# Optimization experiments

Measured on AMD Instinct MI355X. Metric: run time of the kernel, lower is better.

Reference implementation:

```python
import jax, jax.numpy as jnp
import numpy as np

EPS = 1e-8
LRELU_SLOPE = 0.2
ACT_GAIN = float(np.sqrt(2.0))  # def_gain for lrelu
GAIN = 1.0                      # forward default
CLAMP = 256.0


def setup_inputs() -> dict:
    key = jax.random.key(0)
    k1, k2 = jax.random.split(key)
    x = jax.random.normal(k1, (8, 128, 32, 32, 32), dtype=jnp.float32)
    weight = jax.random.normal(k2, (128, 128, 3, 3, 3), dtype=jnp.float32)
    bias = jnp.zeros((128,), dtype=jnp.float32)
    return {"x": x, "weight": weight, "bias": bias}


def _modulated_conv3d(x, weight, styles, padding, demodulate=True):
    # x: [B, Cin, D, H, W], weight: [Cout, Cin, kd, kh, kw], styles: [B, Cin]
    w = weight[None] * styles[:, None, :, None, None, None]  # [B, Cout, Cin, kd, kh, kw]
    if demodulate:
        dcoefs = jax.lax.rsqrt(jnp.sum(jnp.square(w), axis=(2, 3, 4, 5)) + EPS)  # [B, Cout]
        w = w * dcoefs[:, :, None, None, None, None]
    pad = [(padding, padding)] * 3

    def per_sample(xi, wi):
        # xi: [Cin, D, H, W], wi: [Cout, Cin, kd, kh, kw]
        return jax.lax.conv_general_dilated(
            xi[None], wi, window_strides=(1, 1, 1), padding=pad,
            dimension_numbers=("NCDHW", "OIDHW", "NCDHW"))[0]

    return jax.vmap(per_sample)(x, w)  # [B, Cout, D, H, W]


def reference(x, weight, bias):
    padding = weight.shape[-1] // 2
    styles = jnp.ones((x.shape[0], weight.shape[1]), dtype=x.dtype)
    y = _modulated_conv3d(x, weight, styles, padding)
    y = jax.nn.leaky_relu(y + bias[None, :, None, None, None], LRELU_SLOPE)
    # clamp_gain(act, act_gain*gain, 256*gain)
    return jnp.clip(y * (ACT_GAIN * GAIN), -CLAMP * GAIN, CLAMP * GAIN)
```

## Files before the change

### kernel.cpp

```cpp
#include <hip/hip_runtime.h>

typedef short bf16x8 __attribute__((ext_vector_type(8)));
typedef float f32x4  __attribute__((ext_vector_type(4)));
typedef unsigned short u16;

static __device__ __forceinline__ u16 f2bf(float f) {
    unsigned int u = __builtin_bit_cast(unsigned int, f);
    u += 0x7FFFu + ((u >> 16) & 1u);
    return (u16)(u >> 16);
}

static __device__ __forceinline__ void gload_lds16(const void* g, void* l) {
    __builtin_amdgcn_global_load_lds((const __attribute__((address_space(1))) void*)g,
                                     (__attribute__((address_space(3))) void*)l, 16, 0, 0);
}

__global__ __launch_bounds__(256) void prep_w_k(const float* __restrict__ w,
                                                u16* __restrict__ wn) {
    const int co = blockIdx.x;
    const int t  = threadIdx.x;
    const float* wc = w + co * 3456;
    float s = 0.f;
    for (int i = t; i < 3456; i += 256) { float v = wc[i]; s += v * v; }
#pragma unroll
    for (int off = 32; off; off >>= 1) s += __shfl_down(s, off);
    __shared__ float red[4];
    __shared__ float dsh;
    if ((t & 63) == 0) red[t >> 6] = s;
    __syncthreads();
    if (t == 0) dsh = rsqrtf(red[0] + red[1] + red[2] + red[3] + 1e-8f);
    __syncthreads();
    const float d = dsh;
    for (int i = t; i < 3456; i += 256) {
        int ci = i / 27, tap = i - ci * 27;
        float v = wc[i] * d;
        wn[((tap * 4 + (ci >> 5)) * 128 + co) * 32 + (ci & 31)] = f2bf(v);
    }
}

__global__ __launch_bounds__(256) void xpose_k(const float* __restrict__ x,
                                               u16* __restrict__ xt) {
    const int bid = blockIdx.x;
    const int b = bid >> 10, d = (bid >> 5) & 31, h = bid & 31;
    const int t = threadIdx.x;
    const int w = t & 31, cg = t >> 5;
    const int base_dhw = d * 1024 + h * 32 + w;
#pragma unroll
    for (int r = 0; r < 2; ++r) {
        int g = cg + r * 8;
        const float* src = x + ((size_t)(b * 128 + g * 8) << 15) + base_dhw;
        bf16x8 pk;
#pragma unroll
        for (int j = 0; j < 8; ++j) pk[j] = (short)f2bf(src[(size_t)j << 15]);
        *(bf16x8*)&xt[((size_t)((b * 16 + g) << 15) + base_dhw) * 8] = pk;
    }
}

#define KSX 1048576
#define KSW 4096
__global__ __launch_bounds__(512, 4) void conv_mx(
    const u16* __restrict__ wsb, const float* __restrict__ bias,
    float* __restrict__ out) {
    __shared__ __align__(16) u16 lds[24576];
    const u16* xt = wsb + 524288;
    const u16* wn = wsb + 512;
    const u16* zp = wsb;

    const int t = threadIdx.x, lane = t & 63, wid = t >> 6;
    const int ll = lane & 15, g = lane >> 4;
    const int mslice = wid >> 1, ncol = wid & 1;

    int wg = ((blockIdx.x & 7) << 7) | (blockIdx.x >> 3);
    const int b = wg >> 7, dt = (wg >> 3) & 15, ht = wg & 7;
    const int d0 = dt * 2, h0 = ht * 4;

    const int pos0 = mslice * 64 + ll;
    const int xro = pos0 * 32 + ((g ^ ((pos0 >> 1) & 3)) * 8);
    const int co0 = ncol * 64 + ll;
    const int wro = 16384 + co0 * 32 + ((g ^ ((co0 >> 1) & 3)) * 8);

    const int posA = wid * 32 + (lane >> 2);
    const int slot = lane & 3;
    const int pdA = posA >> 7, phA = (posA >> 5) & 3, wA = posA & 31;
    const int gA = slot ^ ((posA >> 1) & 3);
    const int wco = wid * 16 + (lane >> 2);
    const u16* wsrc = wn + wco * 32 + ((slot ^ ((wco >> 1) & 3)) * 8);

    f32x4 acc[4][4];
#pragma unroll
    for (int i = 0; i < 4; ++i)
#pragma unroll
        for (int j = 0; j < 4; ++j) acc[i][j] = (f32x4){0.f, 0.f, 0.f, 0.f};

    const u16* xs0; bool okA, okB;
    const u16* xn0; bool nkA, nkB;

#define MKADDR(OD, OH, OW, A0, OA, OB) { \
    int Dx = d0 + pdA - 1 + (OD), Hx = h0 + phA - 1 + (OH), Wx = wA - 1 + (OW); \
    bool dh_ = ((unsigned)Dx < 32u) && ((unsigned)Hx < 32u); \
    OA = dh_ && ((unsigned)Wx < 32u); \
    OB = dh_ && (Wx < 16); \
    A0 = xt + (long)((b * 16 + gA) * 32768 + Dx * 1024 + Hx * 32 + Wx) * 8; }

#define STAGE(A0, OA, OB, PAR) { \
    gload_lds16(OA ? (const void*)(A0) : (const void*)zp, (void*)&lds[(PAR)*8192 + wid*1024]); \
    gload_lds16(OB ? (const void*)((A0) + 128) : (const void*)zp, (void*)&lds[(PAR)*8192 + wid*1024 + 512]); \
    gload_lds16((const void*)wsrc, (void*)&lds[16384 + (PAR)*4096 + wid*512]); \
    A0 += KSX; wsrc += KSW; }

#define FRAGMFMA(PAR) { \
    bf16x8 xf[4], wf[4]; \
    _Pragma("unroll") for (int mf = 0; mf < 4; ++mf) \
        xf[mf] = *(const bf16x8*)&lds[xro + (PAR)*8192 + mf*512]; \
    _Pragma("unroll") for (int nf = 0; nf < 4; ++nf) \
        wf[nf] = *(const bf16x8*)&lds[wro + (PAR)*4096 + nf*512]; \
    __builtin_amdgcn_s_setprio(1); \
    _Pragma("unroll") for (int mf = 0; mf < 4; ++mf) \
    _Pragma("unroll") for (int nf = 0; nf < 4; ++nf) \
        acc[mf][nf] = __builtin_amdgcn_mfma_f32_16x16x32_bf16(wf[nf], xf[mf], acc[mf][nf], 0, 0, 0); \
    __builtin_amdgcn_s_setprio(0); }

    MKADDR(0, 0, 0, xs0, okA, okB);
    STAGE(xs0, okA, okB, 0);
    __syncthreads();

    for (int od = 0; od < 3; ++od)
    for (int oh = 0; oh < 3; ++oh)
    for (int ow = 0; ow < 3; ++ow) {
        const bool last = (od == 2) && (oh == 2) && (ow == 2);
        STAGE(xs0, okA, okB, 1);
        FRAGMFMA(0);
        __syncthreads();
        STAGE(xs0, okA, okB, 0);
        {
            int own = (ow < 2) ? ow + 1 : 0;
            int ohn = (ow < 2) ? oh : ((oh < 2) ? oh + 1 : 0);
            int odn = (ow < 2) ? od : ((oh < 2) ? od : od + 1);
            MKADDR(odn, ohn, own, xn0, nkA, nkB);
        }
        FRAGMFMA(1);
        __syncthreads();
        STAGE(xs0, okA, okB, 1);
        FRAGMFMA(0);
        __syncthreads();
        if (!last) { STAGE(xn0, nkA, nkB, 0); }
        FRAGMFMA(1);
        __syncthreads();
        xs0 = xn0; okA = nkA; okB = nkB;
    }

    const int pd = mslice >> 1, phb = (mslice & 1) * 2;
#pragma unroll
    for (int nf = 0; nf < 4; ++nf) {
        f32x4 bb = *(const f32x4*)&bias[ncol * 64 + nf * 16 + g * 4];
#pragma unroll
        for (int mf = 0; mf < 4; ++mf) {
            const int wq = (mf & 1) * 16 + ll;
            const int hh = h0 + phb + (mf >> 1);
            float* orow = out + ((size_t)(b * 128 + ncol * 64 + nf * 16 + g * 4) << 15)
                          + (d0 + pd) * 1024 + hh * 32 + wq;
#pragma unroll
            for (int q = 0; q < 4; ++q) {
                float v = acc[mf][nf][q] + bb[q];
                v = v > 0.f ? v : v * 0.2f;
                v *= 1.41421356237f;
                v = fminf(fmaxf(v, -256.f), 256.f);
                orow[(size_t)q << 15] = v;
            }
        }
    }
#undef MKADDR
#undef STAGE
#undef FRAGMFMA
}

#define NPOS 544
__global__ __launch_bounds__(256, 4) void conv_fb(
    const float* __restrict__ x, const u16* __restrict__ wn,
    const float* __restrict__ bias, float* __restrict__ out) {
    __shared__ __align__(16) u16 lds[NPOS * 32];
    float* ldsf = reinterpret_cast<float*>(lds);
    const int t = threadIdx.x;
    const int lane = t & 63;
    const int wid  = t >> 6;
    const int wr   = wid >> 1;
    const int wcn  = wid & 1;
    const int ll   = lane & 15;
    const int g    = lane >> 4;
    const int bid = blockIdx.x;
    const int b  = bid >> 8;
    const int dt = (bid >> 4) & 15, ht = bid & 15;
    const int d0 = dt * 2, h0 = ht * 2;
    const int sw  = t & 31;
    const int sg  = (t >> 5) & 3;
    const int rhi = t >> 7;
    f32x4 acc[4][4];
#pragma unroll
    for (int i = 0; i < 4; ++i)
#pragma unroll
        for (int j = 0; j < 4; ++j) acc[i][j] = (f32x4){0.f, 0.f, 0.f, 0.f};
    float bv[4][4];
#pragma unroll
    for (int nf = 0; nf < 4; ++nf) {
        f32x4 bb = *(const f32x4*)&bias[wcn * 64 + nf * 16 + g * 4];
#pragma unroll
        for (int q = 0; q < 4; ++q) bv[nf][q] = bb[q];
    }
    if (t < 128) {
        int pi  = t >> 2;
        int row = pi >> 1;
        int pos = row * 34 + (pi & 1) * 33;
        bf16x8 z = {0, 0, 0, 0, 0, 0, 0, 0};
        *(bf16x8*)&lds[pos * 32 + (t & 3) * 8] = z;
    }
    for (int c = 0; c < 4; ++c) {
        if (c) __syncthreads();
#pragma unroll
        for (int p = 0; p < 8; ++p) {
            int rowid = p * 2 + rhi;
            int pd = rowid >> 2, ph = rowid & 3;
            int d = d0 - 1 + pd, h = h0 - 1 + ph;
            bool ok = ((unsigned)d < 32u) && ((unsigned)h < 32u);
            const float* src = x + (((b * 128 + c * 32 + sg * 8) * 32 + d) * 32 + h) * 32 + sw;
            float v[8];
#pragma unroll
            for (int j = 0; j < 8; ++j) v[j] = ok ? src[j * 32768] : 0.f;
            bf16x8 pk;
#pragma unroll
            for (int j = 0; j < 8; ++j) pk[j] = (short)f2bf(v[j]);
            int pos = rowid * 34 + sw + 1;
            int sl = sg ^ ((pos >> 1) & 3);
            *(bf16x8*)&lds[pos * 32 + sl * 8] = pk;
        }
        __syncthreads();
        const u16* wbase = wn + c * 4096 + ((wcn * 64 + ll) * 32 + g * 8);
        bf16x8 wf[4];
#pragma unroll
        for (int nf = 0; nf < 4; ++nf) wf[nf] = *(const bf16x8*)&wbase[nf * 512];
#pragma unroll
        for (int tap = 0; tap < 27; ++tap) {
            const int od = tap / 9, oh = (tap / 3) % 3, ow = tap % 3;
            bf16x8 wfn[4];
            if (tap < 26) {
#pragma unroll
                for (int nf = 0; nf < 4; ++nf)
                    wfn[nf] = *(const bf16x8*)&wbase[(tap + 1) * 16384 + nf * 512];
            }
            bf16x8 xf[4];
#pragma unroll
            for (int mf = 0; mf < 4; ++mf) {
                int pos = ((wr + od) * 4 + (mf >> 1) + oh) * 34 + (mf & 1) * 16 + ll + ow;
                int sl = g ^ ((pos >> 1) & 3);
                xf[mf] = *(const bf16x8*)&lds[pos * 32 + sl * 8];
            }
            __builtin_amdgcn_s_setprio(1);
#pragma unroll
            for (int mf = 0; mf < 4; ++mf)
#pragma unroll
                for (int nf = 0; nf < 4; ++nf)
                    acc[mf][nf] = __builtin_amdgcn_mfma_f32_16x16x32_bf16(
                        wf[nf], xf[mf], acc[mf][nf], 0, 0, 0);
            __builtin_amdgcn_s_setprio(0);
            if (tap < 26) {
#pragma unroll
                for (int nf = 0; nf < 4; ++nf) wf[nf] = wfn[nf];
            }
        }
    }
#pragma unroll
    for (int p = 0; p < 4; ++p) {
        const int dd = p >> 1, hh = p & 1;
        __syncthreads();
        if (wr == dd) {
#pragma unroll
            for (int whalf = 0; whalf < 2; ++whalf) {
                const int mf = hh * 2 + whalf;
#pragma unroll
                for (int nf = 0; nf < 4; ++nf) {
#pragma unroll
                    for (int q = 0; q < 4; ++q) {
                        const int co = wcn * 64 + nf * 16 + g * 4 + q;
                        float v = acc[mf][nf][q] + bv[nf][q];
                        v = v > 0.f ? v : v * 0.2f;
                        v *= 1.41421356237f;
                        v = fminf(fmaxf(v, -256.f), 256.f);
                        ldsf[co * 33 + whalf * 16 + ll] = v;
                    }
                }
            }
        }
        __syncthreads();
#pragma unroll
        for (int it = 0; it < 4; ++it) {
            const int row = it * 32 + (t >> 3);
            const int ls  = t & 7;
            f32x4 v = *(f32x4*)&ldsf[row * 33 + ls * 4];
            *(f32x4*)&out[(size_t)(b * 128 + row) * 32768 +
                          (d0 + dd) * 1024 + (h0 + hh) * 32 + ls * 4] = v;
        }
    }
}

extern "C" void kernel_launch(void* const* d_in, const int* in_sizes, int n_in,
                              void* d_out, int out_size, void* d_ws, size_t ws_size,
                              hipStream_t stream) {
    const float* x    = (const float*)d_in[0];
    const float* w    = (const float*)d_in[1];
    const float* bias = (const float*)d_in[2];
    float* out        = (float*)d_out;
    u16* wsb          = (u16*)d_ws;

    hipMemsetAsync(d_ws, 0, 1024, stream);
    prep_w_k<<<128, 256, 0, stream>>>(w, wsb + 512);

    if (ws_size >= 68157440ull) {
        xpose_k<<<8192, 256, 0, stream>>>(x, wsb + 524288);
        conv_mx<<<1024, 512, 0, stream>>>(wsb, bias, out);
    } else {
        conv_fb<<<2048, 256, 0, stream>>>(x, wsb + 512, bias, out);
    }
}
```

Measured before the change: 343.8 us.

## Triple-buffer conv LDS stages with one barrier per k-step and vmcnt waits

Replaces the double-buffered staging loop, which had a full __syncthreads after every MFMA block, with a three-buffer rotating pipeline. Each k-step waits only on the older outstanding loads (vmcnt 3) and then issues a single raw s_barrier. The loads for the next-next stage are issued right after the fragment reads, so global-to-LDS traffic overlaps more with MFMA work. LDS use per block grows from 48KB to 72KB, which may lower occupancy below the requested 4 blocks per CU. Address recomputation moves into a counter-driven stage macro.

```diff
diff --git a/kernel.cpp b/kernel.cpp
--- a/kernel.cpp
+++ b/kernel.cpp
@@ -58,10 +58,11 @@
 
 #define KSX 1048576
 #define KSW 4096
+#define RB  12288
 __global__ __launch_bounds__(512, 4) void conv_mx(
     const u16* __restrict__ wsb, const float* __restrict__ bias,
     float* __restrict__ out) {
-    __shared__ __align__(16) u16 lds[24576];
+    __shared__ __align__(16) u16 lds[3 * RB];
     const u16* xt = wsb + 524288;
     const u16* wn = wsb + 512;
     const u16* zp = wsb;
@@ -77,7 +78,7 @@
     const int pos0 = mslice * 64 + ll;
     const int xro = pos0 * 32 + ((g ^ ((pos0 >> 1) & 3)) * 8);
     const int co0 = ncol * 64 + ll;
-    const int wro = 16384 + co0 * 32 + ((g ^ ((co0 >> 1) & 3)) * 8);
+    const int wro = co0 * 32 + ((g ^ ((co0 >> 1) & 3)) * 8);
 
     const int posA = wid * 32 + (lane >> 2);
     const int slot = lane & 3;
@@ -92,62 +93,49 @@
 #pragma unroll
         for (int j = 0; j < 4; ++j) acc[i][j] = (f32x4){0.f, 0.f, 0.f, 0.f};
 
-    const u16* xs0; bool okA, okB;
-    const u16* xn0; bool nkA, nkB;
-
-#define MKADDR(OD, OH, OW, A0, OA, OB) { \
-    int Dx = d0 + pdA - 1 + (OD), Hx = h0 + phA - 1 + (OH), Wx = wA - 1 + (OW); \
-    bool dh_ = ((unsigned)Dx < 32u) && ((unsigned)Hx < 32u); \
-    OA = dh_ && ((unsigned)Wx < 32u); \
-    OB = dh_ && (Wx < 16); \
-    A0 = xt + (long)((b * 16 + gA) * 32768 + Dx * 1024 + Hx * 32 + Wx) * 8; }
-
-#define STAGE(A0, OA, OB, PAR) { \
-    gload_lds16(OA ? (const void*)(A0) : (const void*)zp, (void*)&lds[(PAR)*8192 + wid*1024]); \
-    gload_lds16(OB ? (const void*)((A0) + 128) : (const void*)zp, (void*)&lds[(PAR)*8192 + wid*1024 + 512]); \
-    gload_lds16((const void*)wsrc, (void*)&lds[16384 + (PAR)*4096 + wid*512]); \
-    A0 += KSX; wsrc += KSW; }
-
-#define FRAGMFMA(PAR) { \
+    int od_s = 0, oh_s = 0, ow_s = 0, cc_s = 0;
+    const u16* xsA = xt; bool okA = false, okB = false;
+
+#define DO_STAGE(SB) { \
+    if (cc_s == 0) { \
+        int Dx = d0 + pdA - 1 + od_s, Hx = h0 + phA - 1 + oh_s, Wx = wA - 1 + ow_s; \
+        bool dh_ = ((unsigned)Dx < 32u) && ((unsigned)Hx < 32u); \
+        okA = dh_ && ((unsigned)Wx < 32u); \
+        okB = dh_ && (Wx < 16); \
+        xsA = xt + (long)((b * 16 + gA) * 32768 + Dx * 1024 + Hx * 32 + Wx) * 8; } \
+    gload_lds16(okA ? (const void*)xsA : (const void*)zp, (void*)&lds[(SB)*RB + wid*1024]); \
+    gload_lds16(okB ? (const void*)(xsA + 128) : (const void*)zp, (void*)&lds[(SB)*RB + wid*1024 + 512]); \
+    gload_lds16((const void*)wsrc, (void*)&lds[(SB)*RB + 8192 + wid*512]); \
+    xsA += KSX; wsrc += KSW; \
+    if (++cc_s == 4) { cc_s = 0; \
+        if (++ow_s == 3) { ow_s = 0; if (++oh_s == 3) { oh_s = 0; ++od_s; } } } }
+
+#define KSTEP(CB, SB, VMN, DOST) { \
+    asm volatile("s_waitcnt vmcnt(" #VMN ")" ::: "memory"); \
+    asm volatile("s_barrier" ::: "memory"); \
     bf16x8 xf[4], wf[4]; \
     _Pragma("unroll") for (int mf = 0; mf < 4; ++mf) \
-        xf[mf] = *(const bf16x8*)&lds[xro + (PAR)*8192 + mf*512]; \
+        xf[mf] = *(const bf16x8*)&lds[(CB)*RB + xro + mf*512]; \
     _Pragma("unroll") for (int nf = 0; nf < 4; ++nf) \
-        wf[nf] = *(const bf16x8*)&lds[wro + (PAR)*4096 + nf*512]; \
+        wf[nf] = *(const bf16x8*)&lds[(CB)*RB + 8192 + wro + nf*512]; \
+    if (DOST) DO_STAGE(SB); \
     __builtin_amdgcn_s_setprio(1); \
     _Pragma("unroll") for (int mf = 0; mf < 4; ++mf) \
     _Pragma("unroll") for (int nf = 0; nf < 4; ++nf) \
         acc[mf][nf] = __builtin_amdgcn_mfma_f32_16x16x32_bf16(wf[nf], xf[mf], acc[mf][nf], 0, 0, 0); \
     __builtin_amdgcn_s_setprio(0); }
 
-    MKADDR(0, 0, 0, xs0, okA, okB);
-    STAGE(xs0, okA, okB, 0);
-    __syncthreads();
-
-    for (int od = 0; od < 3; ++od)
-    for (int oh = 0; oh < 3; ++oh)
-    for (int ow = 0; ow < 3; ++ow) {
-        const bool last = (od == 2) && (oh == 2) && (ow == 2);
-        STAGE(xs0, okA, okB, 1);
-        FRAGMFMA(0);
-        __syncthreads();
-        STAGE(xs0, okA, okB, 0);
-        {
-            int own = (ow < 2) ? ow + 1 : 0;
-            int ohn = (ow < 2) ? oh : ((oh < 2) ? oh + 1 : 0);
-            int odn = (ow < 2) ? od : ((oh < 2) ? od : od + 1);
-            MKADDR(odn, ohn, own, xn0, nkA, nkB);
-        }
-        FRAGMFMA(1);
-        __syncthreads();
-        STAGE(xs0, okA, okB, 1);
-        FRAGMFMA(0);
-        __syncthreads();
-        if (!last) { STAGE(xn0, nkA, nkB, 0); }
-        FRAGMFMA(1);
-        __syncthreads();
-        xs0 = xn0; okA = nkA; okB = nkB;
-    }
+    DO_STAGE(0);
+    DO_STAGE(1);
+
+    for (int m = 0; m < 35; ++m) {
+        KSTEP(0, 2, 3, 1);
+        KSTEP(1, 0, 3, 1);
+        KSTEP(2, 1, 3, 1);
+    }
+    KSTEP(0, 2, 3, 1);
+    KSTEP(1, 0, 3, 0);
+    KSTEP(2, 0, 0, 0);
 
     const int pd = mslice >> 1, phb = (mslice & 1) * 2;
 #pragma unroll
@@ -169,9 +157,8 @@
             }
         }
     }
-#undef MKADDR
-#undef STAGE
-#undef FRAGMFMA
+#undef DO_STAGE
+#undef KSTEP
 }
 
 #define NPOS 544
```

Result: faster. 296.2 us (-13.8%).
